# Kernel tuning notes

Hardware: AMD Instinct MI355X
Metric: run time of the kernel (lower is better)

## Reference

```python
import jax, jax.numpy as jnp
import numpy as np

NUM_HEADS = 6
DIM = 384            # internal attention dim (MultiHeadAttention default)
IN_DIM = 768
HIDDEN = 3072        # int(in_dim * mlp_ratio)
EPS = 1e-5


def _ln(x, w, b):
    m = x.mean(-1, keepdims=True)
    v = ((x - m) ** 2).mean(-1, keepdims=True)
    return (x - m) / jnp.sqrt(v + EPS) * w + b


def _mha(q_in, c_in, Wq, Wkv, Wp, bp):
    # q_in: [b, n, IN_DIM], c_in: [b, m, IN_DIM]
    b, n, _ = q_in.shape
    m = c_in.shape[1]
    h, d = NUM_HEADS, DIM // NUM_HEADS
    scale = d ** -0.5
    q = (q_in @ Wq).reshape(b, n, h, d)
    kv = (c_in @ Wkv).reshape(b, m, 2, h, d)
    k, v = kv[:, :, 0], kv[:, :, 1]
    attn = jax.nn.softmax(jnp.einsum('bnhd,bmhd->bhnm', q, k) * scale, axis=-1)
    out = jnp.einsum('bhnm,bmhd->bnhd', attn, v).reshape(b, n, DIM)
    return out @ Wp + bp


def _mlp(x, W1, b1, W2, b2):
    return jax.nn.gelu(x @ W1 + b1, approximate=False) @ W2 + b2


def setup_inputs() -> dict:
    key = jax.random.key(0)
    ks = jax.random.split(key, 16)
    s = 0.02
    inp = {
        'query': jax.random.normal(ks[0], (8, 1024, IN_DIM), jnp.float32),
        'context': jax.random.normal(ks[1], (8, 2048, IN_DIM), jnp.float32),
        'ln_w': jnp.ones((IN_DIM,), jnp.float32),
        'ln_b': jnp.zeros((IN_DIM,), jnp.float32),
        'a1_wq': jax.random.normal(ks[2], (IN_DIM, DIM), jnp.float32) * s,
        'a1_wkv': jax.random.normal(ks[3], (IN_DIM, 2 * DIM), jnp.float32) * s,
        'a1_wp': jax.random.normal(ks[4], (DIM, IN_DIM), jnp.float32) * s,
        'a1_bp': jnp.zeros((IN_DIM,), jnp.float32),
        'm1_w1': jax.random.normal(ks[5], (IN_DIM, HIDDEN), jnp.float32) * s,
        'm1_b1': jnp.zeros((HIDDEN,), jnp.float32),
        'm1_w2': jax.random.normal(ks[6], (HIDDEN, IN_DIM), jnp.float32) * s,
        'm1_b2': jnp.zeros((IN_DIM,), jnp.float32),
        'a2_wq': jax.random.normal(ks[7], (IN_DIM, DIM), jnp.float32) * s,
        'a2_wkv': jax.random.normal(ks[8], (IN_DIM, 2 * DIM), jnp.float32) * s,
        'a2_wp': jax.random.normal(ks[9], (DIM, IN_DIM), jnp.float32) * s,
        'a2_bp': jnp.zeros((IN_DIM,), jnp.float32),
        'm2_w1': jax.random.normal(ks[10], (IN_DIM, HIDDEN), jnp.float32) * s,
        'm2_b1': jnp.zeros((HIDDEN,), jnp.float32),
        'm2_w2': jax.random.normal(ks[11], (HIDDEN, IN_DIM), jnp.float32) * s,
        'm2_b2': jnp.zeros((IN_DIM,), jnp.float32),
    }
    return inp


def reference(query, context, ln_w, ln_b,
              a1_wq, a1_wkv, a1_wp, a1_bp,
              m1_w1, m1_b1, m1_w2, m1_b2,
              a2_wq, a2_wkv, a2_wp, a2_bp,
              m2_w1, m2_b1, m2_w2, m2_b2):
    q = _ln(query, ln_w, ln_b)                                   # [b, nq, in_dim]
    c = _mha(q, _ln(context, ln_w, ln_b), a1_wq, a1_wkv, a1_wp, a1_bp)  # [b, nq, in_dim]
    c = c + _mlp(_ln(c, ln_w, ln_b), m1_w1, m1_b1, m1_w2, m1_b2)
    c = c + _mha(q, _ln(c, ln_w, ln_b), a2_wq, a2_wkv, a2_wp, a2_bp)
    c = c + _mlp(_ln(c, ln_w, ln_b), m2_w1, m2_b1, m2_w2, m2_b2)
    return (c, q)
```

## Files before the change

### kernel.cpp

```cpp
#include <hip/hip_runtime.h>
#include <hip/hip_bf16.h>
#include <math.h>

typedef unsigned short u16;
typedef __bf16 bf16x8 __attribute__((ext_vector_type(8)));
typedef short s16x4 __attribute__((ext_vector_type(4)));
typedef float f32x4 __attribute__((ext_vector_type(4)));

#define B_   8
#define NQ   1024
#define NC   2048
#define IND  768
#define DIM  384
#define NH   6
#define HD   64
#define HID  3072

__device__ __forceinline__ u16 f2b(float f){
  unsigned int x = __float_as_uint(f);
  return (u16)((x + 0x7fffu + ((x >> 16) & 1u)) >> 16);
}

__device__ __forceinline__ void gl_lds16(const u16* g, u16* l){
  __builtin_amdgcn_global_load_lds(
    (const __attribute__((address_space(1))) unsigned int*)g,
    (__attribute__((address_space(3))) unsigned int*)l, 16, 0, 0);
}

__global__ void wtrans_kernel(const float* __restrict__ W, u16* __restrict__ Wt,
                              int K, int N){
  __shared__ float tile[32][33];
  int n0 = blockIdx.x * 32, k0 = blockIdx.y * 32;
  int tx = threadIdx.x, ty = threadIdx.y;
  #pragma unroll
  for(int i=0;i<4;i++) tile[ty*4+i][tx] = W[(size_t)(k0+ty*4+i)*N + n0 + tx];
  __syncthreads();
  #pragma unroll
  for(int i=0;i<4;i++) Wt[(size_t)(n0+ty*4+i)*K + k0 + tx] = f2b(tile[tx][ty*4+i]);
}

__global__ void vtrans_kernel(const u16* __restrict__ KV, u16* __restrict__ Vt, int M){
  __shared__ u16 t[64][72];
  int bh = blockIdx.y; int b = bh / NH, h = bh % NH;
  int m0 = blockIdx.x * 64;
  int tx = threadIdx.x & 63, ty = threadIdx.x >> 6;
  #pragma unroll
  for(int i=0;i<16;i++){
    int mm = ty*16+i;
    t[mm][tx] = KV[(size_t)(b*M + m0 + mm)*(2*DIM) + DIM + h*HD + tx];
  }
  __syncthreads();
  #pragma unroll
  for(int i=0;i<16;i++){
    int dd = ty*16+i;
    Vt[(size_t)(bh*HD + dd)*M + m0 + tx] = t[tx][dd];
  }
}

template<bool ALSO_F32>
__global__ void ln_kernel(const float* __restrict__ x, const float* __restrict__ w,
                          const float* __restrict__ bia, u16* __restrict__ yb,
                          float* __restrict__ yf){
  int row = blockIdx.x;
  const float* xr = x + (size_t)row * IND;
  int t = threadIdx.x;
  float v[3];
  v[0] = xr[t]; v[1] = xr[t+256]; v[2] = xr[t+512];
  float s  = v[0]+v[1]+v[2];
  float sq = v[0]*v[0]+v[1]*v[1]+v[2]*v[2];
  #pragma unroll
  for(int o=1;o<64;o<<=1){ s += __shfl_xor(s, o, 64); sq += __shfl_xor(sq, o, 64); }
  __shared__ float ss[4], ssq[4];
  int wid = t >> 6;
  if((t&63)==0){ ss[wid]=s; ssq[wid]=sq; }
  __syncthreads();
  s  = ss[0]+ss[1]+ss[2]+ss[3];
  sq = ssq[0]+ssq[1]+ssq[2]+ssq[3];
  float mean = s * (1.0f/IND);
  float var  = sq * (1.0f/IND) - mean*mean;
  float rs   = rsqrtf(var + 1e-5f);
  #pragma unroll
  for(int i=0;i<3;i++){
    int idx = t + i*256;
    float y = (v[i]-mean)*rs*w[idx] + bia[idx];
    yb[(size_t)row*IND + idx] = f2b(y);
    if(ALSO_F32) yf[(size_t)row*IND + idx] = y;
  }
}

template<int TN, int OUTM, bool BIAS, bool GELU_>
__global__ __launch_bounds__(256) void gemm_bt(const u16* __restrict__ A,
    const u16* __restrict__ Wt, const float* __restrict__ bias,
    void* __restrict__ C, int K, int N){
  constexpr int JT = TN / 32;
  __shared__ __align__(16) u16 As[128][32];
  __shared__ __align__(16) u16 Bs[TN][32];
  int rowblk = blockIdx.x * 128, colblk = blockIdx.y * TN;
  int tid = threadIdx.x;
  int lane = tid & 63, wv = tid >> 6;
  int wm = (wv >> 1) * 64, wn = (wv & 1) * (16*JT);
  int l16 = lane & 15, quad = lane >> 4;
  f32x4 acc[4][JT] = {};
  int sr = lane >> 2;
  int sc = (((lane & 3) ^ ((lane >> 3) & 3)) * 8);
  int rc = ((quad ^ ((l16 >> 1) & 3)) * 8);
  const u16* Ap = A  + (size_t)(rowblk + wv*16 + sr) * K + sc;
  const u16* Bp = Wt + (size_t)(colblk + wv*16 + sr) * K + sc;
  u16* lA0 = &As[wv*16][0];      u16* lA1 = &As[64 + wv*16][0];
  u16* lB0 = &Bs[wv*16][0];
  for(int kt = 0; kt < K; kt += 32){
    gl_lds16(Ap + kt,                 lA0);
    gl_lds16(Ap + (size_t)64*K + kt,  lA1);
    gl_lds16(Bp + kt,                 lB0);
    if(TN == 128){
      gl_lds16(Bp + (size_t)64*K + kt, &Bs[0][0] + (64 + wv*16)*32);
    }
    __syncthreads();
    bf16x8 af[4], bfr[JT];
    #pragma unroll
    for(int i=0;i<4;i++)  af[i]  = *(const bf16x8*)&As[wm + i*16 + l16][rc];
    #pragma unroll
    for(int j=0;j<JT;j++) bfr[j] = *(const bf16x8*)&Bs[wn + j*16 + l16][rc];
    #pragma unroll
    for(int i=0;i<4;i++)
      #pragma unroll
      for(int j=0;j<JT;j++)
        acc[i][j] = __builtin_amdgcn_mfma_f32_16x16x32_bf16(af[i], bfr[j], acc[i][j], 0, 0, 0);
    __syncthreads();
  }
  #pragma unroll
  for(int i=0;i<4;i++){
    #pragma unroll
    for(int j=0;j<JT;j++){
      int grow = rowblk + wm + i*16 + quad*4;
      int gcol = colblk + wn + j*16 + l16;
      float bv = BIAS ? bias[gcol] : 0.0f;
      #pragma unroll
      for(int rg=0; rg<4; rg++){
        float vval = acc[i][j][rg] + bv;
        if(GELU_) vval = 0.5f * vval * (1.0f + erff(vval * 0.70710678118f));
        size_t idx = (size_t)(grow + rg) * N + gcol;
        if(OUTM == 0)      ((u16*)C)[idx]   = f2b(vval);
        else if(OUTM == 1) ((float*)C)[idx] = vval;
        else               ((float*)C)[idx] += vval;
      }
    }
  }
}

__global__ __launch_bounds__(256) void attn_kernel(const u16* __restrict__ Q,
    const u16* __restrict__ KV, const u16* __restrict__ Vtg,
    u16* __restrict__ AO, int M){
  __shared__ __align__(16) u16 Ks[128][68];
  __shared__ __align__(16) u16 Vs[64][132];
  int tid = threadIdx.x, lane = tid & 63, wv = tid >> 6;
  int bh = blockIdx.x % (B_*NH);
  int qt = blockIdx.x / (B_*NH);
  int h = bh % NH, b = bh / NH;
  int l16 = lane & 15, quad = lane >> 4;
  const float sc2 = 0.18033688011f;

  s16x4 qf[4];
  const u16* qp = Q + (size_t)(b*NQ + qt*64 + wv*16 + l16) * DIM + h*HD + quad*4;
  #pragma unroll
  for(int s=0;s<4;s++) qf[s] = *(const s16x4*)(qp + s*16);

  f32x4 o[4] = {};
  float lacc = 0.f;

  for(int cb = 0; cb < M; cb += 128){
    __syncthreads();
    #pragma unroll
    for(int it=0; it<4; it++){
      int idx = tid + it*256;
      int row = idx >> 3, c8 = (idx & 7) * 8;
      *(int4*)&Ks[row][c8] =
        *(const int4*)(KV + (size_t)(b*M + cb + row)*(2*DIM) + h*HD + c8);
    }
    #pragma unroll
    for(int it=0; it<4; it++){
      int idx = tid + it*256;
      int dd = idx >> 4, c8 = (idx & 15) * 8;
      *(int4*)&Vs[dd][c8] =
        *(const int4*)(Vtg + (size_t)(bh*HD + dd)*M + cb + c8);
    }
    __syncthreads();

    s16x4 pp[8];
    #pragma unroll
    for(int cc=0; cc<8; cc++){
      f32x4 z = {};
      #pragma unroll
      for(int s=0;s<4;s++){
        s16x4 kf = *(const s16x4*)&Ks[cc*16 + l16][quad*4 + s*16];
        z = __builtin_amdgcn_mfma_f32_16x16x16bf16_1k(kf, qf[s], z, 0,0,0);
      }
      f32x4 p;
      #pragma unroll
      for(int j=0;j<4;j++) p[j] = exp2f(z[j]*sc2);
      lacc += (p[0]+p[1]) + (p[2]+p[3]);
      s16x4 pb;
      #pragma unroll
      for(int j=0;j<4;j++) pb[j] = (short)f2b(p[j]);
      pp[cc] = pb;
    }
    #pragma unroll
    for(int dn=0;dn<4;dn++){
      #pragma unroll
      for(int t=0;t<8;t++){
        s16x4 vf = *(const s16x4*)&Vs[dn*16 + l16][quad*4 + t*16];
        o[dn] = __builtin_amdgcn_mfma_f32_16x16x16bf16_1k(vf, pp[t], o[dn], 0,0,0);
      }
    }
  }

  lacc += __shfl_xor(lacc, 16, 64);
  lacc += __shfl_xor(lacc, 32, 64);
  float rl = 1.0f / lacc;

  u16* aop = AO + (size_t)(b*NQ + qt*64 + wv*16 + l16) * DIM + h*HD + quad*4;
  #pragma unroll
  for(int dn=0;dn<4;dn++){
    s16x4 ob;
    #pragma unroll
    for(int r=0;r<4;r++) ob[r] = (short)f2b(o[dn][r] * rl);
    *(s16x4*)(aop + dn*16) = ob;
  }
}

extern "C" void kernel_launch(void* const* d_in, const int* in_sizes, int n_in,
                              void* d_out, int out_size, void* d_ws, size_t ws_size,
                              hipStream_t stream){
  const float* query   = (const float*)d_in[0];
  const float* context = (const float*)d_in[1];
  const float* ln_w  = (const float*)d_in[2];
  const float* ln_b  = (const float*)d_in[3];
  const float* a1_wq = (const float*)d_in[4];
  const float* a1_wkv= (const float*)d_in[5];
  const float* a1_wp = (const float*)d_in[6];
  const float* a1_bp = (const float*)d_in[7];
  const float* m1_w1 = (const float*)d_in[8];
  const float* m1_b1 = (const float*)d_in[9];
  const float* m1_w2 = (const float*)d_in[10];
  const float* m1_b2 = (const float*)d_in[11];
  const float* a2_wq = (const float*)d_in[12];
  const float* a2_wkv= (const float*)d_in[13];
  const float* a2_wp = (const float*)d_in[14];
  const float* a2_bp = (const float*)d_in[15];
  const float* m2_w1 = (const float*)d_in[16];
  const float* m2_b1 = (const float*)d_in[17];
  const float* m2_w2 = (const float*)d_in[18];
  const float* m2_b2 = (const float*)d_in[19];
  (void)in_sizes; (void)n_in; (void)out_size; (void)ws_size;

  float* c_out = (float*)d_out;
  float* q_out = c_out + (size_t)B_*NQ*IND;

  char* base = (char*)d_ws;
  size_t off = 0;
  auto alloc = [&](size_t elems)->u16*{
    u16* p = (u16*)(base + off);
    off += ((elems*2) + 255) & ~(size_t)255;
    return p;
  };
  u16* wq1t  = alloc((size_t)DIM*IND);
  u16* wkv1t = alloc((size_t)2*DIM*IND);
  u16* wp1t  = alloc((size_t)IND*DIM);
  u16* w11t  = alloc((size_t)HID*IND);
  u16* w21t  = alloc((size_t)IND*HID);
  u16* wq2t  = alloc((size_t)DIM*IND);
  u16* wkv2t = alloc((size_t)2*DIM*IND);
  u16* wp2t  = alloc((size_t)IND*DIM);
  u16* w12t  = alloc((size_t)HID*IND);
  u16* w22t  = alloc((size_t)IND*HID);
  u16* qn_b  = alloc((size_t)B_*NQ*IND);
  u16* cn_b  = alloc((size_t)B_*NC*IND);
  u16* Tb    = alloc((size_t)B_*NQ*IND);
  u16* Qb    = alloc((size_t)B_*NQ*DIM);
  u16* KVb   = alloc((size_t)B_*NC*2*DIM);
  u16* AOb   = alloc((size_t)B_*NQ*DIM);
  u16* Hb    = alloc((size_t)B_*NQ*HID);
  u16* Vtb   = Hb;

  dim3 tb(32,8);
  wtrans_kernel<<<dim3(DIM/32,   IND/32), tb, 0, stream>>>(a1_wq,  wq1t,  IND, DIM);
  wtrans_kernel<<<dim3(2*DIM/32, IND/32), tb, 0, stream>>>(a1_wkv, wkv1t, IND, 2*DIM);
  wtrans_kernel<<<dim3(IND/32,   DIM/32), tb, 0, stream>>>(a1_wp,  wp1t,  DIM, IND);
  wtrans_kernel<<<dim3(HID/32,   IND/32), tb, 0, stream>>>(m1_w1,  w11t,  IND, HID);
  wtrans_kernel<<<dim3(IND/32,   HID/32), tb, 0, stream>>>(m1_w2,  w21t,  HID, IND);
  wtrans_kernel<<<dim3(DIM/32,   IND/32), tb, 0, stream>>>(a2_wq,  wq2t,  IND, DIM);
  wtrans_kernel<<<dim3(2*DIM/32, IND/32), tb, 0, stream>>>(a2_wkv, wkv2t, IND, 2*DIM);
  wtrans_kernel<<<dim3(IND/32,   DIM/32), tb, 0, stream>>>(a2_wp,  wp2t,  DIM, IND);
  wtrans_kernel<<<dim3(HID/32,   IND/32), tb, 0, stream>>>(m2_w1,  w12t,  IND, HID);
  wtrans_kernel<<<dim3(IND/32,   HID/32), tb, 0, stream>>>(m2_w2,  w22t,  HID, IND);

  ln_kernel<true ><<<B_*NQ, 256, 0, stream>>>(query,   ln_w, ln_b, qn_b, q_out);
  ln_kernel<false><<<B_*NC, 256, 0, stream>>>(context, ln_w, ln_b, cn_b, nullptr);

  gemm_bt<64,0,false,false><<<dim3(B_*NQ/128, DIM/64),  256, 0, stream>>>(qn_b, wq1t,  nullptr, Qb,  IND, DIM);
  gemm_bt<128,0,false,false><<<dim3(B_*NC/128, 2*DIM/128), 256, 0, stream>>>(cn_b, wkv1t, nullptr, KVb, IND, 2*DIM);
  vtrans_kernel<<<dim3(NC/64, B_*NH), 256, 0, stream>>>(KVb, Vtb, NC);
  attn_kernel<<<B_*NH*(NQ/64), 256, 0, stream>>>(Qb, KVb, Vtb, AOb, NC);
  gemm_bt<64,1,true,false><<<dim3(B_*NQ/128, IND/64), 256, 0, stream>>>(AOb, wp1t, a1_bp, c_out, DIM, IND);
  ln_kernel<false><<<B_*NQ, 256, 0, stream>>>(c_out, ln_w, ln_b, Tb, nullptr);
  gemm_bt<128,0,true,true ><<<dim3(B_*NQ/128, HID/128), 256, 0, stream>>>(Tb, w11t, m1_b1, Hb, IND, HID);
  gemm_bt<64,2,true,false><<<dim3(B_*NQ/128, IND/64), 256, 0, stream>>>(Hb, w21t, m1_b2, c_out, HID, IND);
  ln_kernel<false><<<B_*NQ, 256, 0, stream>>>(c_out, ln_w, ln_b, Tb, nullptr);
  gemm_bt<64,0,false,false><<<dim3(B_*NQ/128, DIM/64),  256, 0, stream>>>(qn_b, wq2t,  nullptr, Qb,  IND, DIM);
  gemm_bt<64,0,false,false><<<dim3(B_*NQ/128, 2*DIM/64), 256, 0, stream>>>(Tb,   wkv2t, nullptr, KVb, IND, 2*DIM);
  vtrans_kernel<<<dim3(NQ/64, B_*NH), 256, 0, stream>>>(KVb, Vtb, NQ);
  attn_kernel<<<B_*NH*(NQ/64), 256, 0, stream>>>(Qb, KVb, Vtb, AOb, NQ);
  gemm_bt<64,2,true,false><<<dim3(B_*NQ/128, IND/64), 256, 0, stream>>>(AOb, wp2t, a2_bp, c_out, DIM, IND);
  ln_kernel<false><<<B_*NQ, 256, 0, stream>>>(c_out, ln_w, ln_b, Tb, nullptr);
  gemm_bt<128,0,true,true ><<<dim3(B_*NQ/128, HID/128), 256, 0, stream>>>(Tb, w12t, m2_b1, Hb, IND, HID);
  gemm_bt<64,2,true,false><<<dim3(B_*NQ/128, IND/64), 256, 0, stream>>>(Hb, w22t, m2_b2, c_out, HID, IND);
}
```

Measured before the change: 763.2 us.

## Triple-buffer GEMM LDS tiles with async global-to-LDS prefetch pipeline

```diff
diff --git a/kernel.cpp b/kernel.cpp
--- a/kernel.cpp
+++ b/kernel.cpp
@@ -93,8 +93,8 @@
     const u16* __restrict__ Wt, const float* __restrict__ bias,
     void* __restrict__ C, int K, int N){
   constexpr int JT = TN / 32;
-  __shared__ __align__(16) u16 As[128][32];
-  __shared__ __align__(16) u16 Bs[TN][32];
+  __shared__ __align__(16) u16 As[3][128][32];
+  __shared__ __align__(16) u16 Bs[3][TN][32];
   int rowblk = blockIdx.x * 128, colblk = blockIdx.y * TN;
   int tid = threadIdx.x;
   int lane = tid & 63, wv = tid >> 6;
@@ -106,28 +106,61 @@
   int rc = ((quad ^ ((l16 >> 1) & 3)) * 8);
   const u16* Ap = A  + (size_t)(rowblk + wv*16 + sr) * K + sc;
   const u16* Bp = Wt + (size_t)(colblk + wv*16 + sr) * K + sc;
-  u16* lA0 = &As[wv*16][0];      u16* lA1 = &As[64 + wv*16][0];
-  u16* lB0 = &Bs[wv*16][0];
-  for(int kt = 0; kt < K; kt += 32){
-    gl_lds16(Ap + kt,                 lA0);
-    gl_lds16(Ap + (size_t)64*K + kt,  lA1);
-    gl_lds16(Bp + kt,                 lB0);
-    if(TN == 128){
-      gl_lds16(Bp + (size_t)64*K + kt, &Bs[0][0] + (64 + wv*16)*32);
-    }
-    __syncthreads();
+
+  auto stage = [&](int step, int bi){
+    int kt = step * 32;
+    gl_lds16(Ap + kt,                 &As[bi][wv*16][0]);
+    gl_lds16(Ap + (size_t)64*K + kt,  &As[bi][64 + wv*16][0]);
+    gl_lds16(Bp + kt,                 &Bs[bi][wv*16][0]);
+    if constexpr (TN == 128)
+      gl_lds16(Bp + (size_t)64*K + kt, &Bs[bi][64 + wv*16][0]);
+  };
+  auto compute = [&](int bi){
     bf16x8 af[4], bfr[JT];
     #pragma unroll
-    for(int i=0;i<4;i++)  af[i]  = *(const bf16x8*)&As[wm + i*16 + l16][rc];
-    #pragma unroll
-    for(int j=0;j<JT;j++) bfr[j] = *(const bf16x8*)&Bs[wn + j*16 + l16][rc];
+    for(int i=0;i<4;i++)  af[i]  = *(const bf16x8*)&As[bi][wm + i*16 + l16][rc];
+    #pragma unroll
+    for(int j=0;j<JT;j++) bfr[j] = *(const bf16x8*)&Bs[bi][wn + j*16 + l16][rc];
     #pragma unroll
     for(int i=0;i<4;i++)
       #pragma unroll
       for(int j=0;j<JT;j++)
         acc[i][j] = __builtin_amdgcn_mfma_f32_16x16x32_bf16(af[i], bfr[j], acc[i][j], 0, 0, 0);
-    __syncthreads();
-  }
+  };
+
+  int nt = K / 32;
+  stage(0, 0); stage(1, 1); stage(2, 2);
+
+  int bi = 0;
+  for(int t = 0; t < nt - 3; ++t){
+    if constexpr (TN == 128) asm volatile("s_waitcnt vmcnt(8)" ::: "memory");
+    else                     asm volatile("s_waitcnt vmcnt(6)" ::: "memory");
+    __builtin_amdgcn_s_barrier();
+    __builtin_amdgcn_sched_barrier(0);
+    compute(bi);
+    __builtin_amdgcn_sched_barrier(0);
+    asm volatile("" ::: "memory");
+    __builtin_amdgcn_s_barrier();
+    stage(t + 3, bi);
+    bi = (bi == 2) ? 0 : bi + 1;
+  }
+  if constexpr (TN == 128) asm volatile("s_waitcnt vmcnt(8)" ::: "memory");
+  else                     asm volatile("s_waitcnt vmcnt(6)" ::: "memory");
+  __builtin_amdgcn_s_barrier();
+  __builtin_amdgcn_sched_barrier(0);
+  compute(bi); bi = (bi == 2) ? 0 : bi + 1;
+
+  if constexpr (TN == 128) asm volatile("s_waitcnt vmcnt(4)" ::: "memory");
+  else                     asm volatile("s_waitcnt vmcnt(3)" ::: "memory");
+  __builtin_amdgcn_s_barrier();
+  __builtin_amdgcn_sched_barrier(0);
+  compute(bi); bi = (bi == 2) ? 0 : bi + 1;
+
+  asm volatile("s_waitcnt vmcnt(0)" ::: "memory");
+  __builtin_amdgcn_s_barrier();
+  __builtin_amdgcn_sched_barrier(0);
+  compute(bi);
+
   #pragma unroll
   for(int i=0;i<4;i++){
     #pragma unroll
```

Result: faster. 740.6 us (-3.0%).
